# Optimization experiments

Hardware: AMD Instinct MI355X
Metric: run time of the kernel (lower is better)

Reference implementation:

```python
import jax, jax.numpy as jnp
import numpy as np

D_MODEL = 1024
N_EXPERTS = 16
TOP_K = 2
EXPERT_DIM = 1024
SHARED_DIM = 2048
B, T = 2, 1024


def setup_inputs() -> dict:
    key = jax.random.key(0)
    ks = jax.random.split(key, 7)
    std = 0.02
    return {
        "x": jax.random.normal(ks[0], (B, T, D_MODEL), dtype=jnp.float32),
        "router_w": jax.random.normal(ks[1], (N_EXPERTS, D_MODEL), dtype=jnp.float32) * std,
        "gate_up_w": jax.random.normal(ks[2], (N_EXPERTS, D_MODEL, 2 * EXPERT_DIM), dtype=jnp.float32) * std,
        "down_w": jax.random.normal(ks[3], (N_EXPERTS, EXPERT_DIM, D_MODEL), dtype=jnp.float32) * std,
        "shared_gate_w": jax.random.normal(ks[4], (SHARED_DIM, D_MODEL), dtype=jnp.float32) * std,
        "shared_up_w": jax.random.normal(ks[5], (SHARED_DIM, D_MODEL), dtype=jnp.float32) * std,
        "shared_down_w": jax.random.normal(ks[6], (D_MODEL, SHARED_DIM), dtype=jnp.float32) * std,
    }


def reference(x, router_w, gate_up_w, down_w, shared_gate_w, shared_up_w, shared_down_w):
    Bb, Tt, C = x.shape
    N = Bb * Tt
    E = gate_up_w.shape[0]

    # Router: top-k logits, sigmoid gating (matches torch.topk then sigmoid).
    logits = jnp.einsum('btc,ec->bte', x, router_w)          # [B,T,E]
    top_vals, top_idx = jax.lax.top_k(logits, TOP_K)          # [B,T,K]
    gates = jax.nn.sigmoid(top_vals)

    xf = x.reshape(N, C)
    sel = top_idx.reshape(N, TOP_K)
    gw = gates.reshape(N, TOP_K)

    # Dense per-token expert gate [N,E]: zero except selected experts.
    # top_k indices are distinct per token, so scatter-add == scatter-set.
    w_full = jnp.zeros((N, E), dtype=x.dtype).at[jnp.arange(N)[:, None], sel].add(gw)

    # Run every token through every expert densely (same math as the
    # per-token gather + bmm + scatter_add combine, without materializing
    # [N*K, C, 2H] gathered weight tensors).
    gu = jnp.einsum('nc,ech->neh', xf, gate_up_w)             # [N,E,2H]
    gate, up = jnp.split(gu, 2, axis=-1)
    h = jax.nn.silu(gate) * up                                # [N,E,H]
    out_all = jnp.einsum('neh,ehc->nec', h, down_w)           # [N,E,C]
    moe = jnp.einsum('ne,nec->nc', w_full, out_all).reshape(Bb, Tt, C)

    # Shared expert (SwiGLU MLP).
    sg = jnp.einsum('btc,sc->bts', x, shared_gate_w)
    su = jnp.einsum('btc,sc->bts', x, shared_up_w)
    shared = jnp.einsum('bts,cs->btc', jax.nn.silu(sg) * su, shared_down_w)

    return moe + shared
```

## Files before the change

kernel.cpp:

```cpp
#include <hip/hip_runtime.h>
#include <cstdint>

#define N_TOK 2048
#define CDIM  1024
#define NEXP  16
#define TOPK  2
#define HDIM  1024
#define SDIM  2048
#define ESLOT 48
#define GU_EXP_BLOCKS (ESLOT * 16)
#define GU_SH_BLOCKS  (16 * 32)
#define GU_NWG (GU_EXP_BLOCKS + GU_SH_BLOCKS)
#define DN_EXP_BLOCKS (ESLOT * 8)
#define DN_SH_BLOCKS  (16 * 8)
#define DN_NWG (DN_EXP_BLOCKS + DN_SH_BLOCKS)

typedef __bf16 bf16;
typedef __bf16 bf16x8 __attribute__((ext_vector_type(8)));
typedef float  f32x4  __attribute__((ext_vector_type(4)));
typedef unsigned int u32;
typedef unsigned short u16;

typedef __attribute__((address_space(3))) uint32_t lds_u32_t;
typedef __attribute__((address_space(1))) uint32_t glb_u32_t;

__device__ __forceinline__ void gload16(const void* g, void* l) {
  __builtin_amdgcn_global_load_lds((const glb_u32_t*)(uintptr_t)g,
                                   (lds_u32_t*)(uintptr_t)l, 16, 0, 0);
}
__device__ __forceinline__ float fromb(u16 s) {
  union { float f; u32 u; } z; z.u = ((u32)s) << 16; return z.f;
}
__device__ __forceinline__ int xcd_swz(int bid, int nwg) {
  return (bid & 7) * (nwg >> 3) + (bid >> 3);
}
#define SBAR0() __builtin_amdgcn_sched_barrier(0)
#define WAIT_VM(N) do { asm volatile("s_waitcnt vmcnt(" #N ")" ::: "memory"); \
                        SBAR0(); } while (0)

__global__ void convert_small3(const float* __restrict__ sgw,
                               const float* __restrict__ suw,
                               const float* __restrict__ sdw,
                               bf16* __restrict__ sgw_b,
                               bf16* __restrict__ suw_b,
                               bf16* __restrict__ sdw_b) {
  const int b = blockIdx.x;
  const float* s; bf16* d;
  if (b < 1024)       { s = sgw; d = sgw_b; }
  else if (b < 2048)  { s = suw; d = suw_b; }
  else                { s = sdw; d = sdw_b; }
  int i = ((b & 1023) * 256 + threadIdx.x) * 8;
  float4 f0 = *(const float4*)(s + i);
  float4 f1 = *(const float4*)(s + i + 4);
  bf16x8 v;
  v[0]=(bf16)f0.x; v[1]=(bf16)f0.y; v[2]=(bf16)f0.z; v[3]=(bf16)f0.w;
  v[4]=(bf16)f1.x; v[5]=(bf16)f1.y; v[6]=(bf16)f1.z; v[7]=(bf16)f1.w;
  *(bf16x8*)(d + i) = v;
}

__global__ __launch_bounds__(256)
void convert_t(const float* __restrict__ src, bf16* __restrict__ dst, int K, int N) {
  __shared__ float ld[64 * 68];
  const int e = blockIdx.z;
  const int n0 = blockIdx.x * 64, k0 = blockIdx.y * 64;
  const float* s = src + (size_t)e * K * N;
  bf16* d = dst + (size_t)e * N * K;
  const int t = threadIdx.x;
  const int kk = t >> 4, c4 = (t & 15) * 4;
#pragma unroll
  for (int q = 0; q < 4; ++q) {
    float4 f = *(const float4*)(s + (size_t)(k0 + kk + q * 16) * N + n0 + c4);
    float* lp = &ld[(kk + q * 16) * 68 + c4];
    lp[0] = f.x; lp[1] = f.y; lp[2] = f.z; lp[3] = f.w;
  }
  __syncthreads();
  const int nn = t >> 2, kc = (t & 3) * 16;
  bf16x8 v0, v1;
#pragma unroll
  for (int j = 0; j < 8; ++j) {
    v0[j] = (bf16)ld[(kc + j) * 68 + nn];
    v1[j] = (bf16)ld[(kc + 8 + j) * 68 + nn];
  }
  bf16* dp = d + (size_t)(n0 + nn) * K + k0 + kc;
  *(bf16x8*)dp = v0;
  *(bf16x8*)(dp + 8) = v1;
}

__global__ void router_kernel(const float* __restrict__ x,
                              const float* __restrict__ rw,
                              bf16* __restrict__ xb,
                              int* __restrict__ sel,
                              float* __restrict__ gatew) {
  int n = blockIdx.x;
  int lane = threadIdx.x;
  const float* xr = x + (size_t)n * CDIM;
  float xv[16];
#pragma unroll
  for (int q = 0; q < 4; ++q) {
    float4 f = *(const float4*)(xr + lane * 16 + q * 4);
    xv[q * 4 + 0] = f.x; xv[q * 4 + 1] = f.y; xv[q * 4 + 2] = f.z; xv[q * 4 + 3] = f.w;
  }
  bf16x8 v0, v1;
#pragma unroll
  for (int j = 0; j < 8; ++j) { v0[j] = (bf16)xv[j]; v1[j] = (bf16)xv[8 + j]; }
  bf16* xo = xb + (size_t)n * CDIM + lane * 16;
  *(bf16x8*)xo = v0;
  *(bf16x8*)(xo + 8) = v1;
  float acc[NEXP];
#pragma unroll
  for (int e = 0; e < NEXP; ++e) {
    float a = 0.f;
    const float* rwe = rw + e * CDIM + lane * 16;
#pragma unroll
    for (int j = 0; j < 16; ++j) a += xv[j] * rwe[j];
    acc[e] = a;
  }
#pragma unroll
  for (int off = 32; off > 0; off >>= 1) {
#pragma unroll
    for (int e = 0; e < NEXP; ++e) acc[e] += __shfl_xor(acc[e], off, 64);
  }
  if (lane == 0) {
    int i0 = 0; float v0_ = acc[0];
#pragma unroll
    for (int e = 1; e < NEXP; ++e) if (acc[e] > v0_) { v0_ = acc[e]; i0 = e; }
    int i1 = (i0 == 0) ? 1 : 0; float v1_ = acc[i1];
#pragma unroll
    for (int e = 0; e < NEXP; ++e) if (e != i0 && acc[e] > v1_) { v1_ = acc[e]; i1 = e; }
    sel[2 * n] = i0; sel[2 * n + 1] = i1;
    gatew[2 * n]     = 1.f / (1.f + expf(-v0_));
    gatew[2 * n + 1] = 1.f / (1.f + expf(-v1_));
  }
}

__global__ void scan_scatter(const int* __restrict__ sel,
                             const float* __restrict__ gatew,
                             int* __restrict__ counts,
                             int* __restrict__ offsets,
                             int* __restrict__ tab128,
                             int* __restrict__ ntiles,
                             int* __restrict__ entry_token,
                             float* __restrict__ entry_gate,
                             int* __restrict__ entry_pos) {
  __shared__ int hist[NEXP], cur[NEXP];
  const int t = threadIdx.x;
  if (t < NEXP) hist[t] = 0;
  __syncthreads();
  for (int i = t; i < N_TOK * TOPK; i += 256) atomicAdd(&hist[sel[i]], 1);
  __syncthreads();
  if (t == 0) {
    int s = 0, a = 0;
    for (int e = 0; e < NEXP; ++e) {
      int c = hist[e];
      counts[e] = c; offsets[e] = s; cur[e] = s;
      for (int m0 = 0; m0 < c; m0 += 128) tab128[a++] = (e << 16) | m0;
      s += c;
    }
    ntiles[0] = a;
  }
  __syncthreads();
  for (int i = t; i < N_TOK * TOPK; i += 256) {
    int e = sel[i];
    int pos = atomicAdd(&cur[e], 1);
    entry_token[pos] = i >> 1;
    entry_gate[pos] = gatew[i];
    entry_pos[i] = pos;
  }
}

__global__ __launch_bounds__(512, 2)
void gu9(const bf16* __restrict__ xb,
         const bf16* __restrict__ guwb,
         const bf16* __restrict__ sgwb,
         const bf16* __restrict__ suwb,
         bf16* __restrict__ h_exp,
         bf16* __restrict__ h_sh,
         const int* __restrict__ counts,
         const int* __restrict__ offsets,
         const int* __restrict__ entry_token,
         const int* __restrict__ tab128,
         const int* __restrict__ ntiles) {
  __shared__ __align__(16) bf16 sA[2 * 8192];
  __shared__ __align__(16) bf16 sBg[3 * 4096];
  __shared__ __align__(16) bf16 sBu[3 * 4096];

  const int bid = xcd_swz(blockIdx.x, GU_NWG);
  const int t = threadIdx.x;
  const bool is_exp = bid < GU_EXP_BLOCKS;
  const int wid = t >> 6, lane = t & 63;

  int n0, mguard;
  bf16* hbase; int hstride;
  const bf16 *Bg, *Bu;
  const int arow = t >> 3;
  const int sc = (t & 7) ^ (arow & 7);
  const bf16* asrc[2];

  if (is_exp) {
    const int slot = bid >> 4;
    if (slot >= ntiles[0]) return;
    const int packed = tab128[slot];
    const int e = packed >> 16;
    const int m0 = packed & 0xffff;
    const int cnt = counts[e];
    const int base = offsets[e];
    n0 = (bid & 15) * 64;
    mguard = cnt - m0;
#pragma unroll
    for (int i = 0; i < 2; ++i) {
      int r = m0 + i * 64 + arow;
      int tok = entry_token[base + ((r < cnt) ? r : (cnt - 1))];
      asrc[i] = xb + (size_t)tok * CDIM + sc * 8;
    }
    const bf16* we = guwb + (size_t)e * (2 * HDIM) * CDIM;
    Bg = we + (size_t)n0 * CDIM;
    Bu = we + (size_t)(HDIM + n0) * CDIM;
    hbase = h_exp + (size_t)(base + m0) * HDIM + n0;
    hstride = HDIM;
  } else {
    const int sid = bid - GU_EXP_BLOCKS;
    const int m0 = (sid >> 5) * 128;
    n0 = (sid & 31) * 64;
    mguard = 128;
#pragma unroll
    for (int i = 0; i < 2; ++i)
      asrc[i] = xb + (size_t)(m0 + i * 64 + arow) * CDIM + sc * 8;
    Bg = sgwb + (size_t)n0 * CDIM;
    Bu = suwb + (size_t)n0 * CDIM;
    hbase = h_sh + (size_t)m0 * SDIM + n0;
    hstride = SDIM;
  }

  const int th = t & 255;
  bf16* bdst = (t >= 256) ? sBu : sBg;
  const bf16* Bp = (t >= 256) ? Bu : Bg;
  const bf16* bsrc[2];
#pragma unroll
  for (int i = 0; i < 2; ++i) {
    const int row = i * 32 + (th >> 3);
    const int c = (th & 7) ^ (row & 7);
    bsrc[i] = Bp + (size_t)row * CDIM + c * 8;
  }
  const int adst = t * 8;
  const int bdoff = th * 8;

#define ISSUE_A(k_, ab_)                                                      \
  do {                                                                        \
    _Pragma("unroll")                                                         \
    for (int i = 0; i < 2; ++i)                                               \
      gload16(asrc[i] + (k_), &sA[(ab_) * 8192 + i * 4096 + adst]);           \
  } while (0)
#define ISSUE_B(k_, bo_)                                                      \
  do {                                                                        \
    _Pragma("unroll")                                                         \
    for (int i = 0; i < 2; ++i)                                               \
      gload16(bsrc[i] + (k_), &bdst[(bo_) + i * 2048 + bdoff]);               \
  } while (0)

  const int wr = (wid >> 1) * 32, wc = (wid & 1) * 32;
  const int lrow = lane & 15, grp = lane >> 4;

  f32x4 ag[2][2], au[2][2];
#pragma unroll
  for (int m = 0; m < 2; ++m)
#pragma unroll
    for (int n = 0; n < 2; ++n)
#pragma unroll
      for (int i = 0; i < 4; ++i) { ag[m][n][i] = 0.f; au[m][n][i] = 0.f; }

#define COMPUTE(ab_, bo_)                                                     \
  do {                                                                        \
    _Pragma("unroll")                                                         \
    for (int ks = 0; ks < 2; ++ks) {                                          \
      const int ch = ks * 4 + grp;                                            \
      bf16x8 av[2], bg[2], bu[2];                                             \
      _Pragma("unroll")                                                       \
      for (int m = 0; m < 2; ++m) {                                           \
        const int r = wr + m * 16 + lrow;                                     \
        av[m] = *(const bf16x8*)&sA[(ab_) * 8192 + r * 64 + ((ch ^ (r & 7)) << 3)]; \
      }                                                                       \
      _Pragma("unroll")                                                       \
      for (int n = 0; n < 2; ++n) {                                           \
        const int r = wc + n * 16 + lrow;                                     \
        const int so = r * 64 + ((ch ^ (r & 7)) << 3);                        \
        bg[n] = *(const bf16x8*)&sBg[(bo_) + so];                             \
        bu[n] = *(const bf16x8*)&sBu[(bo_) + so];                             \
      }                                                                       \
      _Pragma("unroll")                                                       \
      for (int m = 0; m < 2; ++m)                                             \
        _Pragma("unroll")                                                     \
        for (int n = 0; n < 2; ++n) {                                         \
          ag[m][n] = __builtin_amdgcn_mfma_f32_16x16x32_bf16(av[m], bg[n], ag[m][n], 0, 0, 0); \
          au[m][n] = __builtin_amdgcn_mfma_f32_16x16x32_bf16(av[m], bu[n], au[m][n], 0, 0, 0); \
        }                                                                     \
    }                                                                         \
  } while (0)

  ISSUE_A(0, 0);
  ISSUE_B(0, 0);
  SBAR0();
  ISSUE_B(64, 4096);
  SBAR0();
  WAIT_VM(2);
  __builtin_amdgcn_s_barrier();

  int bb0 = 0, bb1 = 4096, bb2 = 8192;
  for (int k = 0; k < 14; ++k) {
    ISSUE_A((k + 1) * 64, (k + 1) & 1);
    SBAR0();
    ISSUE_B((k + 2) * 64, bb2);
    SBAR0();
    COMPUTE(k & 1, bb0);
    WAIT_VM(2);
    __builtin_amdgcn_s_barrier();
    int tmp = bb0; bb0 = bb1; bb1 = bb2; bb2 = tmp;
  }
  ISSUE_A(15 * 64, 1);
  SBAR0();
  COMPUTE(0, bb0);
  WAIT_VM(0);
  __builtin_amdgcn_s_barrier();
  { int tmp = bb0; bb0 = bb1; bb1 = bb2; bb2 = tmp; }
  COMPUTE(1, bb0);
#undef ISSUE_A
#undef ISSUE_B
#undef COMPUTE

#pragma unroll
  for (int m = 0; m < 2; ++m) {
#pragma unroll
    for (int i = 0; i < 4; ++i) {
      const int rl = wr + m * 16 + grp * 4 + i;
      if (rl >= mguard) continue;
      bf16* orow = hbase + (size_t)rl * hstride;
#pragma unroll
      for (int n = 0; n < 2; ++n) {
        const float g = ag[m][n][i];
        const float u = au[m][n][i];
        orow[wc + n * 16 + lrow] = (bf16)(g * u * __builtin_amdgcn_rcpf(1.f + __expf(-g)));
      }
    }
  }
}

__global__ __launch_bounds__(512, 2)
void dn9(const bf16* __restrict__ h_exp,
         const bf16* __restrict__ h_sh,
         const bf16* __restrict__ dwb,
         const bf16* __restrict__ sdwb,
         const float* __restrict__ entry_gate,
         bf16* __restrict__ out_e,
         float* __restrict__ out,
         const int* __restrict__ counts,
         const int* __restrict__ offsets,
         const int* __restrict__ tab128,
         const int* __restrict__ ntiles) {
  __shared__ __align__(16) bf16 sA[2 * 8192];
  __shared__ __align__(16) bf16 sB[3 * 8192];

  const int bid = xcd_swz(blockIdx.x, DN_NWG);
  const int t = threadIdx.x;
  const bool is_exp = bid < DN_EXP_BLOCKS;
  const int wid = t >> 6, lane = t & 63;

  int n0, mguard, K, rowbase, NK;
  const bf16* Ab;
  const bf16* Bb;

  if (is_exp) {
    const int slot = bid >> 3;
    if (slot >= ntiles[0]) return;
    const int packed = tab128[slot];
    const int e = packed >> 16;
    const int m0 = packed & 0xffff;
    const int cnt = counts[e];
    n0 = (bid & 7) * 128;
    mguard = cnt - m0;
    K = HDIM; NK = HDIM / 64;
    rowbase = offsets[e] + m0;
    Ab = h_exp;
    Bb = dwb + (size_t)e * CDIM * HDIM + (size_t)n0 * HDIM;
  } else {
    const int sid = bid - DN_EXP_BLOCKS;
    const int m0 = (sid >> 3) * 128;
    n0 = (sid & 7) * 128;
    mguard = 128;
    K = SDIM; NK = SDIM / 64;
    rowbase = m0;
    Ab = h_sh;
    Bb = sdwb + (size_t)n0 * SDIM;
  }

  const int arow = t >> 3;
  const int sc = (t & 7) ^ (arow & 7);
  const bf16* asrc[2];
#pragma unroll
  for (int i = 0; i < 2; ++i) {
    int rg = rowbase + i * 64 + arow;
    if (is_exp && rg > N_TOK * TOPK - 1) rg = N_TOK * TOPK - 1;
    asrc[i] = Ab + (size_t)rg * K + sc * 8;
  }
  const bf16* bsrc[2];
#pragma unroll
  for (int i = 0; i < 2; ++i)
    bsrc[i] = Bb + (size_t)(i * 64 + arow) * K + sc * 8;
  const int adst = t * 8;

#define ISSUE_A(k_, ab_)                                                      \
  do {                                                                        \
    _Pragma("unroll")                                                         \
    for (int i = 0; i < 2; ++i)                                               \
      gload16(asrc[i] + (k_), &sA[(ab_) * 8192 + i * 4096 + adst]);           \
  } while (0)
#define ISSUE_B(k_, bo_)                                                      \
  do {                                                                        \
    _Pragma("unroll")                                                         \
    for (int i = 0; i < 2; ++i)                                               \
      gload16(bsrc[i] + (k_), &sB[(bo_) + i * 4096 + adst]);                  \
  } while (0)

  const int wr = (wid >> 1) * 32, wc = (wid & 1) * 64;
  const int lrow = lane & 15, grp = lane >> 4;

  f32x4 acc[2][4];
#pragma unroll
  for (int m = 0; m < 2; ++m)
#pragma unroll
    for (int n = 0; n < 4; ++n)
#pragma unroll
      for (int i = 0; i < 4; ++i) acc[m][n][i] = 0.f;

#define COMPUTE(ab_, bo_)                                                     \
  do {                                                                        \
    _Pragma("unroll")                                                         \
    for (int ks = 0; ks < 2; ++ks) {                                          \
      const int ch = ks * 4 + grp;                                            \
      bf16x8 av[2], bv[4];                                                    \
      _Pragma("unroll")                                                       \
      for (int m = 0; m < 2; ++m) {                                           \
        const int r = wr + m * 16 + lrow;                                     \
        av[m] = *(const bf16x8*)&sA[(ab_) * 8192 + r * 64 + ((ch ^ (r & 7)) << 3)]; \
      }                                                                       \
      _Pragma("unroll")                                                       \
      for (int n = 0; n < 4; ++n) {                                           \
        const int r = wc + n * 16 + lrow;                                     \
        bv[n] = *(const bf16x8*)&sB[(bo_) + r * 64 + ((ch ^ (r & 7)) << 3)];  \
      }                                                                       \
      _Pragma("unroll")                                                       \
      for (int m = 0; m < 2; ++m)                                             \
        _Pragma("unroll")                                                     \
        for (int n = 0; n < 4; ++n)                                           \
          acc[m][n] = __builtin_amdgcn_mfma_f32_16x16x32_bf16(av[m], bv[n], acc[m][n], 0, 0, 0); \
    }                                                                         \
  } while (0)

  ISSUE_A(0, 0);
  ISSUE_B(0, 0);
  SBAR0();
  ISSUE_B(64, 8192);
  SBAR0();
  WAIT_VM(2);
  __builtin_amdgcn_s_barrier();

  int bb0 = 0, bb1 = 8192, bb2 = 16384;
  for (int k = 0; k < NK - 2; ++k) {
    ISSUE_A((k + 1) * 64, (k + 1) & 1);
    SBAR0();
    ISSUE_B((k + 2) * 64, bb2);
    SBAR0();
    COMPUTE(k & 1, bb0);
    WAIT_VM(2);
    __builtin_amdgcn_s_barrier();
    int tmp = bb0; bb0 = bb1; bb1 = bb2; bb2 = tmp;
  }
  ISSUE_A((NK - 1) * 64, (NK - 1) & 1);
  SBAR0();
  COMPUTE((NK - 2) & 1, bb0);
  WAIT_VM(0);
  __builtin_amdgcn_s_barrier();
  { int tmp = bb0; bb0 = bb1; bb1 = bb2; bb2 = tmp; }
  COMPUTE((NK - 1) & 1, bb0);
#undef ISSUE_A
#undef ISSUE_B
#undef COMPUTE

#pragma unroll
  for (int m = 0; m < 2; ++m) {
#pragma unroll
    for (int i = 0; i < 4; ++i) {
      const int rl = wr + m * 16 + grp * 4 + i;
      if (rl >= mguard) continue;
      if (is_exp) {
        const int row = rowbase + rl;
        const float scl = entry_gate[row];
        bf16* orow = out_e + (size_t)row * CDIM + n0;
#pragma unroll
        for (int n = 0; n < 4; ++n)
          orow[wc + n * 16 + lrow] = (bf16)(acc[m][n][i] * scl);
      } else {
        float* orow = out + (size_t)(rowbase + rl) * CDIM + n0;
#pragma unroll
        for (int n = 0; n < 4; ++n)
          orow[wc + n * 16 + lrow] = acc[m][n][i];
      }
    }
  }
}

__global__ void combine_kernel(float* __restrict__ out,
                               const bf16* __restrict__ out_e,
                               const int* __restrict__ entry_pos) {
  int tid = blockIdx.x * blockDim.x + threadIdx.x;
  int n = tid >> 8;
  int c4 = tid & 255;
  int p0 = entry_pos[2 * n];
  int p1 = entry_pos[2 * n + 1];
  float4 v = ((const float4*)out)[tid];
  ushort4 a = *(const ushort4*)((const u16*)out_e + (size_t)p0 * CDIM + c4 * 4);
  ushort4 b = *(const ushort4*)((const u16*)out_e + (size_t)p1 * CDIM + c4 * 4);
  v.x += fromb(a.x) + fromb(b.x);
  v.y += fromb(a.y) + fromb(b.y);
  v.z += fromb(a.z) + fromb(b.z);
  v.w += fromb(a.w) + fromb(b.w);
  ((float4*)out)[tid] = v;
}

extern "C" void kernel_launch(void* const* d_in, const int* in_sizes, int n_in,
                              void* d_out, int out_size, void* d_ws, size_t ws_size,
                              hipStream_t stream) {
  const float* x   = (const float*)d_in[0];
  const float* rw  = (const float*)d_in[1];
  const float* guw = (const float*)d_in[2];
  const float* dw  = (const float*)d_in[3];
  const float* sgw = (const float*)d_in[4];
  const float* suw = (const float*)d_in[5];
  const float* sdw = (const float*)d_in[6];
  float* out = (float*)d_out;
  char* ws = (char*)d_ws;
  const size_t MB = 1048576;

  int*   sel         = (int*)(ws + 0);
  float* gatew       = (float*)(ws + 16384);
  int*   counts      = (int*)(ws + 32768);
  int*   offsets     = (int*)(ws + 32832);
  int*   ntiles      = (int*)(ws + 32960);
  int*   tab128      = (int*)(ws + 33024);
  int*   entry_token = (int*)(ws + 33664);
  float* entry_gate  = (float*)(ws + 50048);
  int*   entry_pos   = (int*)(ws + 66432);

  bf16* xb    = (bf16*)(ws + 82816);
  bf16* h_exp = (bf16*)(ws + 82816 + 4 * MB);
  bf16* h_sh  = (bf16*)(ws + 82816 + 12 * MB);
  bf16* sgw_b = (bf16*)(ws + 82816 + 20 * MB);
  bf16* suw_b = (bf16*)(ws + 82816 + 24 * MB);
  bf16* Wbig  = (bf16*)(ws + 82816 + 28 * MB);
  bf16* sdw_b = (bf16*)(ws + 82816 + 92 * MB);
  bf16* out_e = sgw_b;

  router_kernel<<<N_TOK, 64, 0, stream>>>(x, rw, xb, sel, gatew);
  scan_scatter<<<1, 256, 0, stream>>>(sel, gatew, counts, offsets, tab128,
                                      ntiles, entry_token, entry_gate, entry_pos);

  convert_t<<<dim3(32, 16, NEXP), 256, 0, stream>>>(guw, Wbig, CDIM, 2 * HDIM);
  convert_small3<<<3072, 256, 0, stream>>>(sgw, suw, sdw, sgw_b, suw_b, sdw_b);

  gu9<<<GU_NWG, 512, 0, stream>>>(xb, Wbig, sgw_b, suw_b, h_exp, h_sh,
                                  counts, offsets, entry_token, tab128, ntiles);

  convert_t<<<dim3(16, 16, NEXP), 256, 0, stream>>>(dw, Wbig, HDIM, CDIM);

  dn9<<<DN_NWG, 512, 0, stream>>>(h_exp, h_sh, Wbig, sdw_b, entry_gate, out_e, out,
                                  counts, offsets, tab128, ntiles);

  combine_kernel<<<(N_TOK * CDIM / 4) / 256, 256, 0, stream>>>(out, out_e, entry_pos);
}
```

Before: 178.0 us.

## Fuse weight conversions and scan into prep kernel; overlap down-weight conversion with gate-up GEMM

Merges scan_scatter, the gate_up weight transpose-convert and the shared-weight conversions into one prep_kernel launch. The down_w transpose-convert now runs as extra blocks appended to the gate-up GEMM grid, so it can overlap with GEMM work. down_w gets its own buffer instead of reusing the gate_up buffer. The router packs four tokens per 256-thread block. The aim is fewer launches and better GPU fill, at the cost of the conversion blocks competing with GEMM blocks for LDS and occupancy.

```diff
diff --git a/kernel.cpp b/kernel.cpp
--- a/kernel.cpp
+++ b/kernel.cpp
@@ -11,9 +11,13 @@
 #define GU_EXP_BLOCKS (ESLOT * 16)
 #define GU_SH_BLOCKS  (16 * 32)
 #define GU_NWG (GU_EXP_BLOCKS + GU_SH_BLOCKS)
+#define DW_CONV_BLOCKS 2048
+#define GU9X_NWG (GU_NWG + DW_CONV_BLOCKS)
 #define DN_EXP_BLOCKS (ESLOT * 8)
 #define DN_SH_BLOCKS  (16 * 8)
 #define DN_NWG (DN_EXP_BLOCKS + DN_SH_BLOCKS)
+#define PREP_GUW_TILES 8192
+#define PREP_NWG (1 + PREP_GUW_TILES + 3072)
 
 typedef __bf16 bf16;
 typedef __bf16 bf16x8 __attribute__((ext_vector_type(8)));
@@ -38,18 +42,143 @@
 #define WAIT_VM(N) do { asm volatile("s_waitcnt vmcnt(" #N ")" ::: "memory"); \
                         SBAR0(); } while (0)
 
-__global__ void convert_small3(const float* __restrict__ sgw,
-                               const float* __restrict__ suw,
-                               const float* __restrict__ sdw,
-                               bf16* __restrict__ sgw_b,
-                               bf16* __restrict__ suw_b,
-                               bf16* __restrict__ sdw_b) {
+__device__ __forceinline__ void conv_tile(const float* __restrict__ s,
+                                          bf16* __restrict__ d,
+                                          int K, int N, int k0, int n0,
+                                          int t, float* ld) {
+  const int kk = t >> 4, c4 = (t & 15) * 4;
+#pragma unroll
+  for (int q = 0; q < 4; ++q) {
+    float4 f = *(const float4*)(s + (size_t)(k0 + kk + q * 16) * N + n0 + c4);
+    float* lp = &ld[(kk + q * 16) * 68 + c4];
+    lp[0] = f.x; lp[1] = f.y; lp[2] = f.z; lp[3] = f.w;
+  }
+  __syncthreads();
+  const int nn = t >> 2, kc = (t & 3) * 16;
+  bf16x8 v0, v1;
+#pragma unroll
+  for (int j = 0; j < 8; ++j) {
+    v0[j] = (bf16)ld[(kc + j) * 68 + nn];
+    v1[j] = (bf16)ld[(kc + 8 + j) * 68 + nn];
+  }
+  bf16* dp = d + (size_t)(n0 + nn) * K + k0 + kc;
+  *(bf16x8*)dp = v0;
+  *(bf16x8*)(dp + 8) = v1;
+}
+
+__global__ __launch_bounds__(256)
+void router_kernel(const float* __restrict__ x,
+                   const float* __restrict__ rw,
+                   bf16* __restrict__ xb,
+                   int* __restrict__ sel,
+                   float* __restrict__ gatew) {
+  int n = blockIdx.x * 4 + (threadIdx.x >> 6);
+  int lane = threadIdx.x & 63;
+  const float* xr = x + (size_t)n * CDIM;
+  float xv[16];
+#pragma unroll
+  for (int q = 0; q < 4; ++q) {
+    float4 f = *(const float4*)(xr + lane * 16 + q * 4);
+    xv[q * 4 + 0] = f.x; xv[q * 4 + 1] = f.y; xv[q * 4 + 2] = f.z; xv[q * 4 + 3] = f.w;
+  }
+  bf16x8 v0, v1;
+#pragma unroll
+  for (int j = 0; j < 8; ++j) { v0[j] = (bf16)xv[j]; v1[j] = (bf16)xv[8 + j]; }
+  bf16* xo = xb + (size_t)n * CDIM + lane * 16;
+  *(bf16x8*)xo = v0;
+  *(bf16x8*)(xo + 8) = v1;
+  float acc[NEXP];
+#pragma unroll
+  for (int e = 0; e < NEXP; ++e) {
+    float a = 0.f;
+    const float* rwe = rw + e * CDIM + lane * 16;
+#pragma unroll
+    for (int j = 0; j < 16; ++j) a += xv[j] * rwe[j];
+    acc[e] = a;
+  }
+#pragma unroll
+  for (int off = 32; off > 0; off >>= 1) {
+#pragma unroll
+    for (int e = 0; e < NEXP; ++e) acc[e] += __shfl_xor(acc[e], off, 64);
+  }
+  if (lane == 0) {
+    int i0 = 0; float v0_ = acc[0];
+#pragma unroll
+    for (int e = 1; e < NEXP; ++e) if (acc[e] > v0_) { v0_ = acc[e]; i0 = e; }
+    int i1 = (i0 == 0) ? 1 : 0; float v1_ = acc[i1];
+#pragma unroll
+    for (int e = 0; e < NEXP; ++e) if (e != i0 && acc[e] > v1_) { v1_ = acc[e]; i1 = e; }
+    sel[2 * n] = i0; sel[2 * n + 1] = i1;
+    gatew[2 * n]     = 1.f / (1.f + expf(-v0_));
+    gatew[2 * n + 1] = 1.f / (1.f + expf(-v1_));
+  }
+}
+
+__global__ __launch_bounds__(256)
+void prep_kernel(const float* __restrict__ guw,
+                 const float* __restrict__ sgw,
+                 const float* __restrict__ suw,
+                 const float* __restrict__ sdw,
+                 bf16* __restrict__ guw_b,
+                 bf16* __restrict__ sgw_b,
+                 bf16* __restrict__ suw_b,
+                 bf16* __restrict__ sdw_b,
+                 const int* __restrict__ sel,
+                 const float* __restrict__ gatew,
+                 int* __restrict__ counts,
+                 int* __restrict__ offsets,
+                 int* __restrict__ tab128,
+                 int* __restrict__ ntiles,
+                 int* __restrict__ entry_token,
+                 float* __restrict__ entry_gate,
+                 int* __restrict__ entry_pos) {
+  __shared__ __align__(16) float ld[64 * 68];
   const int b = blockIdx.x;
+  const int t = threadIdx.x;
+  if (b == 0) {
+    int* hist = (int*)ld;
+    int* cur = hist + NEXP;
+    if (t < NEXP) hist[t] = 0;
+    __syncthreads();
+    for (int i = t; i < N_TOK * TOPK; i += 256) atomicAdd(&hist[sel[i]], 1);
+    __syncthreads();
+    if (t == 0) {
+      int s = 0, a = 0;
+      for (int e = 0; e < NEXP; ++e) {
+        int c = hist[e];
+        counts[e] = c; offsets[e] = s; cur[e] = s;
+        for (int m0 = 0; m0 < c; m0 += 128) tab128[a++] = (e << 16) | m0;
+        s += c;
+      }
+      ntiles[0] = a;
+    }
+    __syncthreads();
+    for (int i = t; i < N_TOK * TOPK; i += 256) {
+      int e = sel[i];
+      int pos = atomicAdd(&cur[e], 1);
+      entry_token[pos] = i >> 1;
+      entry_gate[pos] = gatew[i];
+      entry_pos[i] = pos;
+    }
+    return;
+  }
+  if (b <= PREP_GUW_TILES) {
+    const int idx = b - 1;
+    const int e = idx >> 9;
+    const int rem = idx & 511;
+    const int n0 = (rem & 31) << 6;
+    const int k0 = (rem >> 5) << 6;
+    conv_tile(guw + (size_t)e * CDIM * 2 * HDIM,
+              guw_b + (size_t)e * 2 * HDIM * CDIM,
+              CDIM, 2 * HDIM, k0, n0, t, ld);
+    return;
+  }
+  const int b2 = b - 1 - PREP_GUW_TILES;
   const float* s; bf16* d;
-  if (b < 1024)       { s = sgw; d = sgw_b; }
-  else if (b < 2048)  { s = suw; d = suw_b; }
+  if (b2 < 1024)      { s = sgw; d = sgw_b; }
+  else if (b2 < 2048) { s = suw; d = suw_b; }
   else                { s = sdw; d = sdw_b; }
-  int i = ((b & 1023) * 256 + threadIdx.x) * 8;
+  int i = ((b2 & 1023) * 256 + t) * 8;
   float4 f0 = *(const float4*)(s + i);
   float4 f1 = *(const float4*)(s + i + 4);
   bf16x8 v;
@@ -58,134 +187,41 @@
   *(bf16x8*)(d + i) = v;
 }
 
-__global__ __launch_bounds__(256)
-void convert_t(const float* __restrict__ src, bf16* __restrict__ dst, int K, int N) {
-  __shared__ float ld[64 * 68];
-  const int e = blockIdx.z;
-  const int n0 = blockIdx.x * 64, k0 = blockIdx.y * 64;
-  const float* s = src + (size_t)e * K * N;
-  bf16* d = dst + (size_t)e * N * K;
+__global__ __launch_bounds__(512, 2)
+void gu9x(const bf16* __restrict__ xb,
+          const bf16* __restrict__ guwb,
+          const bf16* __restrict__ sgwb,
+          const bf16* __restrict__ suwb,
+          bf16* __restrict__ h_exp,
+          bf16* __restrict__ h_sh,
+          const int* __restrict__ counts,
+          const int* __restrict__ offsets,
+          const int* __restrict__ entry_token,
+          const int* __restrict__ tab128,
+          const int* __restrict__ ntiles,
+          const float* __restrict__ dw,
+          bf16* __restrict__ dw_b) {
+  __shared__ __align__(16) char smem[81920];
+  bf16* sA  = (bf16*)smem;
+  bf16* sBg = (bf16*)(smem + 32768);
+  bf16* sBu = (bf16*)(smem + 57344);
+
   const int t = threadIdx.x;
-  const int kk = t >> 4, c4 = (t & 15) * 4;
-#pragma unroll
-  for (int q = 0; q < 4; ++q) {
-    float4 f = *(const float4*)(s + (size_t)(k0 + kk + q * 16) * N + n0 + c4);
-    float* lp = &ld[(kk + q * 16) * 68 + c4];
-    lp[0] = f.x; lp[1] = f.y; lp[2] = f.z; lp[3] = f.w;
-  }
-  __syncthreads();
-  const int nn = t >> 2, kc = (t & 3) * 16;
-  bf16x8 v0, v1;
-#pragma unroll
-  for (int j = 0; j < 8; ++j) {
-    v0[j] = (bf16)ld[(kc + j) * 68 + nn];
-    v1[j] = (bf16)ld[(kc + 8 + j) * 68 + nn];
-  }
-  bf16* dp = d + (size_t)(n0 + nn) * K + k0 + kc;
-  *(bf16x8*)dp = v0;
-  *(bf16x8*)(dp + 8) = v1;
-}
-
-__global__ void router_kernel(const float* __restrict__ x,
-                              const float* __restrict__ rw,
-                              bf16* __restrict__ xb,
-                              int* __restrict__ sel,
-                              float* __restrict__ gatew) {
-  int n = blockIdx.x;
-  int lane = threadIdx.x;
-  const float* xr = x + (size_t)n * CDIM;
-  float xv[16];
-#pragma unroll
-  for (int q = 0; q < 4; ++q) {
-    float4 f = *(const float4*)(xr + lane * 16 + q * 4);
-    xv[q * 4 + 0] = f.x; xv[q * 4 + 1] = f.y; xv[q * 4 + 2] = f.z; xv[q * 4 + 3] = f.w;
-  }
-  bf16x8 v0, v1;
-#pragma unroll
-  for (int j = 0; j < 8; ++j) { v0[j] = (bf16)xv[j]; v1[j] = (bf16)xv[8 + j]; }
-  bf16* xo = xb + (size_t)n * CDIM + lane * 16;
-  *(bf16x8*)xo = v0;
-  *(bf16x8*)(xo + 8) = v1;
-  float acc[NEXP];
-#pragma unroll
-  for (int e = 0; e < NEXP; ++e) {
-    float a = 0.f;
-    const float* rwe = rw + e * CDIM + lane * 16;
-#pragma unroll
-    for (int j = 0; j < 16; ++j) a += xv[j] * rwe[j];
-    acc[e] = a;
-  }
-#pragma unroll
-  for (int off = 32; off > 0; off >>= 1) {
-#pragma unroll
-    for (int e = 0; e < NEXP; ++e) acc[e] += __shfl_xor(acc[e], off, 64);
-  }
-  if (lane == 0) {
-    int i0 = 0; float v0_ = acc[0];
-#pragma unroll
-    for (int e = 1; e < NEXP; ++e) if (acc[e] > v0_) { v0_ = acc[e]; i0 = e; }
-    int i1 = (i0 == 0) ? 1 : 0; float v1_ = acc[i1];
-#pragma unroll
-    for (int e = 0; e < NEXP; ++e) if (e != i0 && acc[e] > v1_) { v1_ = acc[e]; i1 = e; }
-    sel[2 * n] = i0; sel[2 * n + 1] = i1;
-    gatew[2 * n]     = 1.f / (1.f + expf(-v0_));
-    gatew[2 * n + 1] = 1.f / (1.f + expf(-v1_));
-  }
-}
-
-__global__ void scan_scatter(const int* __restrict__ sel,
-                             const float* __restrict__ gatew,
-                             int* __restrict__ counts,
-                             int* __restrict__ offsets,
-                             int* __restrict__ tab128,
-                             int* __restrict__ ntiles,
-                             int* __restrict__ entry_token,
-                             float* __restrict__ entry_gate,
-                             int* __restrict__ entry_pos) {
-  __shared__ int hist[NEXP], cur[NEXP];
-  const int t = threadIdx.x;
-  if (t < NEXP) hist[t] = 0;
-  __syncthreads();
-  for (int i = t; i < N_TOK * TOPK; i += 256) atomicAdd(&hist[sel[i]], 1);
-  __syncthreads();
-  if (t == 0) {
-    int s = 0, a = 0;
-    for (int e = 0; e < NEXP; ++e) {
-      int c = hist[e];
-      counts[e] = c; offsets[e] = s; cur[e] = s;
-      for (int m0 = 0; m0 < c; m0 += 128) tab128[a++] = (e << 16) | m0;
-      s += c;
-    }
-    ntiles[0] = a;
-  }
-  __syncthreads();
-  for (int i = t; i < N_TOK * TOPK; i += 256) {
-    int e = sel[i];
-    int pos = atomicAdd(&cur[e], 1);
-    entry_token[pos] = i >> 1;
-    entry_gate[pos] = gatew[i];
-    entry_pos[i] = pos;
-  }
-}
-
-__global__ __launch_bounds__(512, 2)
-void gu9(const bf16* __restrict__ xb,
-         const bf16* __restrict__ guwb,
-         const bf16* __restrict__ sgwb,
-         const bf16* __restrict__ suwb,
-         bf16* __restrict__ h_exp,
-         bf16* __restrict__ h_sh,
-         const int* __restrict__ counts,
-         const int* __restrict__ offsets,
-         const int* __restrict__ entry_token,
-         const int* __restrict__ tab128,
-         const int* __restrict__ ntiles) {
-  __shared__ __align__(16) bf16 sA[2 * 8192];
-  __shared__ __align__(16) bf16 sBg[3 * 4096];
-  __shared__ __align__(16) bf16 sBu[3 * 4096];
+
+  if (blockIdx.x >= GU_NWG) {
+    const int tid2 = (blockIdx.x - GU_NWG) * 2 + (t >> 8);
+    float* ld = (float*)(smem + (t >> 8) * 17408);
+    const int e = tid2 >> 8;
+    const int rem = tid2 & 255;
+    const int n0c = (rem & 15) << 6;
+    const int k0c = (rem >> 4) << 6;
+    conv_tile(dw + (size_t)e * HDIM * CDIM,
+              dw_b + (size_t)e * CDIM * HDIM,
+              HDIM, CDIM, k0c, n0c, t & 255, ld);
+    return;
+  }
 
   const int bid = xcd_swz(blockIdx.x, GU_NWG);
-  const int t = threadIdx.x;
   const bool is_exp = bid < GU_EXP_BLOCKS;
   const int wid = t >> 6, lane = t & 63;
 
@@ -554,23 +590,23 @@
   bf16* h_sh  = (bf16*)(ws + 82816 + 12 * MB);
   bf16* sgw_b = (bf16*)(ws + 82816 + 20 * MB);
   bf16* suw_b = (bf16*)(ws + 82816 + 24 * MB);
-  bf16* Wbig  = (bf16*)(ws + 82816 + 28 * MB);
-  bf16* sdw_b = (bf16*)(ws + 82816 + 92 * MB);
+  bf16* guw_b = (bf16*)(ws + 82816 + 28 * MB);
+  bf16* dw_b  = (bf16*)(ws + 82816 + 92 * MB);
+  bf16* sdw_b = (bf16*)(ws + 82816 + 124 * MB);
   bf16* out_e = sgw_b;
 
-  router_kernel<<<N_TOK, 64, 0, stream>>>(x, rw, xb, sel, gatew);
-  scan_scatter<<<1, 256, 0, stream>>>(sel, gatew, counts, offsets, tab128,
-                                      ntiles, entry_token, entry_gate, entry_pos);
-
-  convert_t<<<dim3(32, 16, NEXP), 256, 0, stream>>>(guw, Wbig, CDIM, 2 * HDIM);
-  convert_small3<<<3072, 256, 0, stream>>>(sgw, suw, sdw, sgw_b, suw_b, sdw_b);
-
-  gu9<<<GU_NWG, 512, 0, stream>>>(xb, Wbig, sgw_b, suw_b, h_exp, h_sh,
-                                  counts, offsets, entry_token, tab128, ntiles);
-
-  convert_t<<<dim3(16, 16, NEXP), 256, 0, stream>>>(dw, Wbig, HDIM, CDIM);
-
-  dn9<<<DN_NWG, 512, 0, stream>>>(h_exp, h_sh, Wbig, sdw_b, entry_gate, out_e, out,
+  router_kernel<<<N_TOK / 4, 256, 0, stream>>>(x, rw, xb, sel, gatew);
+
+  prep_kernel<<<PREP_NWG, 256, 0, stream>>>(guw, sgw, suw, sdw,
+                                            guw_b, sgw_b, suw_b, sdw_b,
+                                            sel, gatew, counts, offsets, tab128,
+                                            ntiles, entry_token, entry_gate, entry_pos);
+
+  gu9x<<<GU9X_NWG, 512, 0, stream>>>(xb, guw_b, sgw_b, suw_b, h_exp, h_sh,
+                                     counts, offsets, entry_token, tab128, ntiles,
+                                     dw, dw_b);
+
+  dn9<<<DN_NWG, 512, 0, stream>>>(h_exp, h_sh, dw_b, sdw_b, entry_gate, out_e, out,
                                   counts, offsets, tab128, ntiles);
 
   combine_kernel<<<(N_TOK * CDIM / 4) / 256, 256, 0, stream>>>(out, out_e, entry_pos);
```

Result: faster. 158.9 us (median of 2 runs) (-10.7%).
